# Optimization experiments

Hardware: AMD Instinct MI355X
Metric: run time of the kernel (lower is better)

Reference implementation:

```python
import jax, jax.numpy as jnp
import numpy as np
import math

N_QUBITS = 8
EMBED_DIM = 8
NUM_HEADS = 2
N_QLAYERS = 2
TWO_PI = 2.0 * math.pi


def _apply_rx(state, theta, wire):
    # state: (N,) + (2,)*n complex64; theta: scalar or (N,)
    n = state.ndim - 1
    ax = 1 + wire
    a0 = jnp.take(state, 0, axis=ax)
    a1 = jnp.take(state, 1, axis=ax)
    half = jnp.asarray(theta) * 0.5
    c = jnp.cos(half)
    s = jnp.sin(half)
    if c.ndim:  # per-sample angle -> broadcast over remaining qubit axes
        bshape = (-1,) + (1,) * (n - 1)
        c = c.reshape(bshape)
        s = s.reshape(bshape)
    js = 1j * s
    n0 = c * a0 - js * a1
    n1 = -js * a0 + c * a1
    return jnp.stack([n0, n1], axis=ax)


def _apply_cnot(state, ctrl, tgt):
    ac, at = 1 + ctrl, 1 + tgt
    s0 = jnp.take(state, 0, axis=ac)
    s1 = jnp.take(state, 1, axis=ac)
    at2 = at - 1 if at > ac else at  # target axis index after removing control axis
    s1 = jnp.flip(s1, axis=at2)
    return jnp.stack([s0, s1], axis=ac)


def qnode(inputs, weights):
    """AngleEmbedding(RX) + BasicEntanglerLayers(RX + CNOT ring), PauliZ expvals.
    inputs: (N, n) angles; weights: (L, n). Returns (N, n) expvals, fully batched."""
    N, n = inputs.shape
    L = weights.shape[0]
    state = jnp.zeros((N,) + (2,) * n, jnp.complex64)
    state = state.at[(slice(None),) + (0,) * n].set(1.0)
    for i in range(n):  # AngleEmbedding: RX(inputs[:, i]) on wire i
        state = _apply_rx(state, inputs[:, i], i)
    for l in range(L):  # BasicEntanglerLayers
        for i in range(n):
            state = _apply_rx(state, weights[l, i], i)
        for i in range(n):
            state = _apply_cnot(state, i, (i + 1) % n)
    probs = (state.real ** 2 + state.imag ** 2).reshape(N, 2 ** n)
    # wire 0 is the most significant bit of the flattened statevector index
    idx = jnp.arange(2 ** n)
    bits = (idx[:, None] >> jnp.arange(n - 1, -1, -1)[None, :]) & 1  # (2^n, n)
    signs = (1.0 - 2.0 * bits).astype(probs.dtype)
    return probs @ signs  # (N, n)


def _qproj(x, weights):
    # apply qnode to every (batch, timestep) vector at once (vectorized loop fusion)
    B, S, E = x.shape
    return qnode(x.reshape(B * S, E), weights).reshape(B, S, E)


def _attention_forward(q, k, v, wq_w, wk_w, wv_w, wd_w):
    B, S, E = q.shape
    H, D = NUM_HEADS, EMBED_DIM // NUM_HEADS
    qp = _qproj(q, wq_w)
    kp = _qproj(k, wk_w)
    vp = _qproj(v, wv_w)
    # split heads: (B, H, S, D)
    qh = qp.reshape(B, S, H, D).transpose(0, 2, 1, 3)
    kh = kp.reshape(B, S, H, D).transpose(0, 2, 1, 3)
    vh = vp.reshape(B, S, H, D).transpose(0, 2, 1, 3)
    scores = jnp.einsum('bhqd,bhkd->bhqk', qh, kh) / jnp.sqrt(jnp.asarray(D, qh.dtype))
    attn = jax.nn.softmax(scores, axis=-1)
    ctx = jnp.einsum('bhqk,bhkd->bhqd', attn, vh)
    concat = ctx.transpose(0, 2, 1, 3).reshape(B, S, E)
    out = _qproj(concat, wd_w)
    return out, attn


def setup_inputs() -> dict:
    key = jax.random.key(0)
    kq, kk, kv, k1, k2, k3, k4 = jax.random.split(key, 7)
    B, S, E = 32, 1024, EMBED_DIM
    return {
        'q': jax.random.normal(kq, (B, S, E), jnp.float32),
        'k': jax.random.normal(kk, (B, S, E), jnp.float32),
        'v': jax.random.normal(kv, (B, S, E), jnp.float32),
        'wq_weights': jax.random.uniform(k1, (N_QLAYERS, N_QUBITS), jnp.float32) * TWO_PI,
        'wk_weights': jax.random.uniform(k2, (N_QLAYERS, N_QUBITS), jnp.float32) * TWO_PI,
        'wv_weights': jax.random.uniform(k3, (N_QLAYERS, N_QUBITS), jnp.float32) * TWO_PI,
        'dense_weights': jax.random.uniform(k4, (N_QLAYERS, N_QUBITS), jnp.float32) * TWO_PI,
    }


def reference(q, k, v, wq_weights, wk_weights, wv_weights, dense_weights):
    return _attention_forward(q, k, v, wq_weights, wk_weights, wv_weights, dense_weights)
```

## Files before the change

kernel.cpp:

```cpp
#include <hip/hip_runtime.h>
#include <math.h>


#define NSAMP 32768

#define QX1 0xB1
#define QX2 0x4E
#define QX3 0x1B
#define QB0 0x00
#define QB1 0x55
#define QB2 0xAA
#define QB3 0xFF
#define ROW_MIRROR 0x140
#define ROW_HALF_MIRROR 0x141

template <int CTRL>
__device__ __forceinline__ float dppf(float x) {
  int xi = __float_as_int(x);
  return __int_as_float(
      __builtin_amdgcn_update_dpp(xi, xi, CTRL, 0xF, 0xF, false));
}

template <int ML>
__device__ __forceinline__ void gate_l(float c, float s, float* ar,
                                       float* ai) {
  constexpr int HB = ML >= 32 ? 32 : ML >= 16 ? 16 : ML >= 8 ? 8
                     : ML >= 4 ? 4 : ML >= 2 ? 2 : 1;
#pragma unroll
  for (int l = 0; l < 64; ++l) {
    if (!(l & HB)) {
      const int p = l ^ ML;
      float a0r = ar[l], a0i = ai[l], a1r = ar[p], a1i = ai[p];
      ar[l] = fmaf(c, a0r, s * a1i);
      ai[l] = fmaf(c, a0i, -s * a1r);
      ar[p] = fmaf(c, a1r, s * a0i);
      ai[p] = fmaf(c, a1i, -s * a0r);
    }
  }
}

template <int CTRL, int ML>
__device__ __forceinline__ void gate_q(float c, float s, float* ar,
                                       float* ai) {
  if constexpr (ML == 0) {
#pragma unroll
    for (int l = 0; l < 64; ++l) {
      float pr = dppf<CTRL>(ar[l]);
      float pi = dppf<CTRL>(ai[l]);
      ar[l] = fmaf(c, ar[l], s * pi);
      ai[l] = fmaf(c, ai[l], -s * pr);
    }
  } else {
    constexpr int HB = ML >= 32 ? 32 : ML >= 16 ? 16 : ML >= 8 ? 8
                       : ML >= 4 ? 4 : ML >= 2 ? 2 : 1;
#pragma unroll
    for (int l = 0; l < 64; ++l) {
      if (!(l & HB)) {
        const int p = l ^ ML;
        float prl = dppf<CTRL>(ar[p]);
        float pil = dppf<CTRL>(ai[p]);
        float prp = dppf<CTRL>(ar[l]);
        float pip = dppf<CTRL>(ai[l]);
        ar[l] = fmaf(c, ar[l], s * pil);
        ai[l] = fmaf(c, ai[l], -s * prl);
        ar[p] = fmaf(c, ar[p], s * pip);
        ai[p] = fmaf(c, ai[p], -s * prp);
      }
    }
  }
}

__device__ __forceinline__ float quad_wht(float v, int qq) {
  float u = dppf<QX1>(v);
  v = (qq & 1) ? (u - v) : (v + u);
  u = dppf<QX2>(v);
  v = (qq & 2) ? (u - v) : (v + u);
  return v;
}

__device__ __forceinline__ void qsim_wave(const float* __restrict__ in,
                                          float* __restrict__ outp,
                                          int sampBase,
                                          const float* __restrict__ wc,
                                          const float* __restrict__ wsn) {
  const int lane = threadIdx.x & 63;
  const int qq = lane & 3;
  const int g = lane >> 2;
  const int samp = sampBase + g;

  const float2 xx = *(const float2*)(in + (size_t)samp * 8 + 2 * qq);
  float h0 = 0.5f * xx.x, h1 = 0.5f * xx.y;
  float c0 = cosf(h0), s0 = sinf(h0);
  float c1 = cosf(h1), s1 = sinf(h1);
  float cw[8], sw[8];
  cw[0] = dppf<QB0>(c0); cw[1] = dppf<QB0>(c1);
  sw[0] = dppf<QB0>(s0); sw[1] = dppf<QB0>(s1);
  cw[2] = dppf<QB1>(c0); cw[3] = dppf<QB1>(c1);
  sw[2] = dppf<QB1>(s0); sw[3] = dppf<QB1>(s1);
  cw[4] = dppf<QB2>(c0); cw[5] = dppf<QB2>(c1);
  sw[4] = dppf<QB2>(s0); sw[5] = dppf<QB2>(s1);
  cw[6] = dppf<QB3>(c0); cw[7] = dppf<QB3>(c1);
  sw[6] = dppf<QB3>(s0); sw[7] = dppf<QB3>(s1);

  float ar[64], ai[64];
  ar[0] = ((qq & 1) ? sw[1] : cw[1]) * ((qq & 2) ? sw[0] : cw[0]);
#pragma unroll
  for (int k = 0; k < 6; ++k) {
    const float cc = cw[7 - k], ss = sw[7 - k];
#pragma unroll
    for (int t = (1 << k) - 1; t >= 0; --t) {
      ar[t + (1 << k)] = ar[t] * ss;
      ar[t] = ar[t] * cc;
    }
  }
  {
    const int pq = __builtin_popcount(qq);
#pragma unroll
    for (int l = 63; l >= 0; --l) {
      const int pl = __builtin_popcount(l) & 3;
      const float mm = ar[l];
      if (pl == 0) { ar[l] = mm;   ai[l] = 0.0f; }
      else if (pl == 1) { ar[l] = 0.0f; ai[l] = -mm; }
      else if (pl == 2) { ar[l] = -mm;  ai[l] = 0.0f; }
      else { ar[l] = 0.0f; ai[l] = mm; }
    }
    if (pq == 1) {
#pragma unroll
      for (int l = 0; l < 64; ++l) {
        const float t = ar[l];
        ar[l] = ai[l];
        ai[l] = -t;
      }
    } else if (pq == 2) {
#pragma unroll
      for (int l = 0; l < 64; ++l) {
        ar[l] = -ar[l];
        ai[l] = -ai[l];
      }
    }
  }

  gate_q<QX2, 0>(wc[0], wsn[0], ar, ai);
  gate_q<QX1, 0>(wc[1], wsn[1], ar, ai);
  gate_l<0x20>(wc[2], wsn[2], ar, ai);
  gate_l<0x10>(wc[3], wsn[3], ar, ai);
  gate_l<0x08>(wc[4], wsn[4], ar, ai);
  gate_l<0x04>(wc[5], wsn[5], ar, ai);
  gate_l<0x02>(wc[6], wsn[6], ar, ai);
  gate_l<0x01>(wc[7], wsn[7], ar, ai);
  gate_q<QX3, 0>(wc[8], wsn[8], ar, ai);
  gate_q<QX1, 0x20>(wc[9], wsn[9], ar, ai);
  gate_l<0x30>(wc[10], wsn[10], ar, ai);
  gate_l<0x18>(wc[11], wsn[11], ar, ai);
  gate_l<0x0C>(wc[12], wsn[12], ar, ai);
  gate_l<0x06>(wc[13], wsn[13], ar, ai);
  gate_l<0x03>(wc[14], wsn[14], ar, ai);
  gate_q<QX3, 0x01>(wc[15], wsn[15], ar, ai);

  float p[64];
#pragma unroll
  for (int l = 0; l < 64; ++l) p[l] = ar[l] * ar[l] + ai[l] * ai[l];
#pragma unroll
  for (int k = 0; k < 6; ++k) {
#pragma unroll
    for (int l = 0; l < 64; ++l) {
      if (!(l & (1 << k))) {
        const int q2 = l | (1 << k);
        const float a = p[l], b = p[q2];
        p[l] = a + b;
        p[q2] = a - b;
      }
    }
  }
  const float o15 = quad_wht(p[0x15], qq);
  const float o3F = quad_wht(p[0x3F], qq);
  const float o1F = quad_wht(p[0x1F], qq);
  const float o2F = quad_wht(p[0x2F], qq);
  const float o17 = quad_wht(p[0x17], qq);
  const float o2B = quad_wht(p[0x2B], qq);
  const float o2A = quad_wht(p[0x2A], qq);

  float* orow = outp + (size_t)samp * 8;
  if (qq == 3) orow[0] = o15;
  if (qq == 2) {
    orow[1] = o3F;
    orow[3] = o2F;
    orow[5] = o2B;
    orow[7] = o2A;
  }
  if (qq == 1) {
    orow[2] = o1F;
    orow[4] = o17;
    orow[6] = o15;
  }
}

__device__ __forceinline__ void weight_trig(const float* __restrict__ w,
                                            float* __restrict__ tc,
                                            float* __restrict__ tsn) {
  if (threadIdx.x < 32) {
    const int a = threadIdx.x & 15;
    const float half = 0.5f * w[a];
    if (threadIdx.x < 16)
      tc[a] = cosf(half);
    else
      tsn[a] = sinf(half);
  }
  __syncthreads();
}

__global__ __launch_bounds__(256, 2) void mhaq_qproj3_kernel(
    const float* __restrict__ q, const float* __restrict__ k,
    const float* __restrict__ v, const float* __restrict__ wq,
    const float* __restrict__ wk, const float* __restrict__ wv,
    float* __restrict__ qp, float* __restrict__ kp, float* __restrict__ vp) {
  __shared__ float tc[16], tsn[16];
  const int wg = blockIdx.x * 4 + (threadIdx.x >> 6);
  const int proj = wg >> 11;
  const float* wsel = proj == 0 ? wq : proj == 1 ? wk : wv;
  weight_trig(wsel, tc, tsn);
  const float* in = proj == 0 ? q : proj == 1 ? k : v;
  float* op = proj == 0 ? qp : proj == 1 ? kp : vp;
  qsim_wave(in, op, (wg & 2047) * 16, tc, tsn);
}

__global__ __launch_bounds__(256, 2) void mhaq_qproj1_kernel(
    const float* __restrict__ ctx, const float* __restrict__ wd,
    float* __restrict__ outp) {
  __shared__ float tc[16], tsn[16];
  weight_trig(wd, tc, tsn);
  const int wg = blockIdx.x * 4 + (threadIdx.x >> 6);
  qsim_wave(ctx, outp, wg * 16, tc, tsn);
}

__device__ __forceinline__ float wred_sum(float v) {
  v += dppf<QX1>(v);
  v += dppf<QX2>(v);
  v += dppf<ROW_HALF_MIRROR>(v);
  v += dppf<ROW_MIRROR>(v);
  v += __shfl_xor(v, 16, 64);
  v += __shfl_xor(v, 32, 64);
  return v;
}
__device__ __forceinline__ float wred_max(float v) {
  v = fmaxf(v, dppf<QX1>(v));
  v = fmaxf(v, dppf<QX2>(v));
  v = fmaxf(v, dppf<ROW_HALF_MIRROR>(v));
  v = fmaxf(v, dppf<ROW_MIRROR>(v));
  v = fmaxf(v, __shfl_xor(v, 16, 64));
  v = fmaxf(v, __shfl_xor(v, 32, 64));
  return v;
}

__global__ __launch_bounds__(256, 2) void mhaq_attn_kernel(
    const float* __restrict__ qp, const float* __restrict__ kp,
    const float* __restrict__ vp, float* __restrict__ ctx,
    float* __restrict__ attn) {
  const int wg = blockIdx.x * 4 + (threadIdx.x >> 6);
  const int bh = wg >> 7;
  const int chunk = wg & 127;
  const int b = bh >> 1, h = bh & 1;
  const int lane = threadIdx.x & 63;

  float4 kreg[16], vreg[16];
  const float* kbase = kp + (size_t)b * 1024 * 8 + h * 4;
  const float* vbase = vp + (size_t)b * 1024 * 8 + h * 4;
#pragma unroll
  for (int t = 0; t < 4; ++t) {
#pragma unroll
    for (int c = 0; c < 4; ++c) {
      const size_t j = (size_t)t * 256 + lane * 4 + c;
      kreg[t * 4 + c] = *(const float4*)(kbase + j * 8);
      vreg[t * 4 + c] = *(const float4*)(vbase + j * 8);
    }
  }

  for (int r = 0; r < 8; ++r) {
    const int i = chunk * 8 + r;
    const float4 qv = *(const float4*)(qp + ((size_t)b * 1024 + i) * 8 + h * 4);
    float e[16];
    float mx = -1e30f;
#pragma unroll
    for (int t = 0; t < 16; ++t) {
      float s = qv.x * kreg[t].x + qv.y * kreg[t].y + qv.z * kreg[t].z +
                qv.w * kreg[t].w;
      s *= 0.5f;
      e[t] = s;
      mx = fmaxf(mx, s);
    }
    mx = wred_max(mx);
    float sum = 0.0f;
#pragma unroll
    for (int t = 0; t < 16; ++t) {
      e[t] = __expf(e[t] - mx);
      sum += e[t];
    }
    sum = wred_sum(sum);
    const float rinv = 1.0f / sum;

    float a0 = 0.f, a1 = 0.f, a2 = 0.f, a3 = 0.f;
    float* arow = attn + ((size_t)(bh * 1024 + i)) * 1024;
#pragma unroll
    for (int t = 0; t < 4; ++t) {
      float p0 = e[4 * t] * rinv, p1 = e[4 * t + 1] * rinv,
            p2 = e[4 * t + 2] * rinv, p3 = e[4 * t + 3] * rinv;
      *(float4*)(arow + t * 256 + lane * 4) = make_float4(p0, p1, p2, p3);
      a0 = fmaf(p0, vreg[4 * t].x, a0);
      a1 = fmaf(p0, vreg[4 * t].y, a1);
      a2 = fmaf(p0, vreg[4 * t].z, a2);
      a3 = fmaf(p0, vreg[4 * t].w, a3);
      a0 = fmaf(p1, vreg[4 * t + 1].x, a0);
      a1 = fmaf(p1, vreg[4 * t + 1].y, a1);
      a2 = fmaf(p1, vreg[4 * t + 1].z, a2);
      a3 = fmaf(p1, vreg[4 * t + 1].w, a3);
      a0 = fmaf(p2, vreg[4 * t + 2].x, a0);
      a1 = fmaf(p2, vreg[4 * t + 2].y, a1);
      a2 = fmaf(p2, vreg[4 * t + 2].z, a2);
      a3 = fmaf(p2, vreg[4 * t + 2].w, a3);
      a0 = fmaf(p3, vreg[4 * t + 3].x, a0);
      a1 = fmaf(p3, vreg[4 * t + 3].y, a1);
      a2 = fmaf(p3, vreg[4 * t + 3].z, a2);
      a3 = fmaf(p3, vreg[4 * t + 3].w, a3);
    }
    a0 = wred_sum(a0);
    a1 = wred_sum(a1);
    a2 = wred_sum(a2);
    a3 = wred_sum(a3);
    if (lane == 0)
      *(float4*)(ctx + ((size_t)b * 1024 + i) * 8 + h * 4) =
          make_float4(a0, a1, a2, a3);
  }
}

extern "C" void kernel_launch(void* const* d_in, const int* in_sizes, int n_in,
                              void* d_out, int out_size, void* d_ws,
                              size_t ws_size, hipStream_t stream) {
  (void)in_sizes; (void)n_in; (void)out_size; (void)ws_size;
  const float* q = (const float*)d_in[0];
  const float* k = (const float*)d_in[1];
  const float* v = (const float*)d_in[2];
  const float* wq = (const float*)d_in[3];
  const float* wk = (const float*)d_in[4];
  const float* wv = (const float*)d_in[5];
  const float* wd = (const float*)d_in[6];
  float* outp = (float*)d_out;
  float* attn = outp + 262144;

  float* wsf = (float*)d_ws;
  float* qp = wsf;
  float* kp = qp + (size_t)NSAMP * 8;
  float* vp = kp + (size_t)NSAMP * 8;
  float* ctx = vp + (size_t)NSAMP * 8;

  hipLaunchKernelGGL(mhaq_qproj3_kernel, dim3(1536), dim3(256), 0, stream, q,
                     k, v, wq, wk, wv, qp, kp, vp);
  hipLaunchKernelGGL(mhaq_attn_kernel, dim3(2048), dim3(256), 0, stream, qp,
                     kp, vp, ctx, attn);
  hipLaunchKernelGGL(mhaq_qproj1_kernel, dim3(512), dim3(256), 0, stream, ctx,
                     wd, outp);
}
```

Measured before the change: 385.5 us.

## Pack statevector into float2 pairs for packed FMA and prune the Walsh-Hadamard

Stores the per-lane 64-amplitude statevector as 32 float2 pairs, with the lowest local qubit held inside each pair, so gate updates can use packed FP32 FMA instructions (v_pk_fma_f32). Gates on that qubit become in-pair swaps. The final Walsh-Hadamard reduction is cut to 3 stages per group of eight, and only the seven needed output coefficients are built explicitly. This is meant to halve the VALU instruction count, at the cost of extra swizzle moves and possible register-allocation changes.

After: 364.7 us. 1.06x faster.

```diff
diff --git a/kernel.cpp b/kernel.cpp
--- a/kernel.cpp
+++ b/kernel.cpp
@@ -3,6 +3,8 @@
 
 
 #define NSAMP 32768
+
+typedef float f2 __attribute__((ext_vector_type(2)));
 
 #define QX1 0xB1
 #define QX2 0x4E
@@ -21,51 +23,101 @@
       __builtin_amdgcn_update_dpp(xi, xi, CTRL, 0xF, 0xF, false));
 }
 
+template <int CTRL>
+__device__ __forceinline__ f2 dpp2(f2 v) {
+  f2 r;
+  r.x = dppf<CTRL>(v.x);
+  r.y = dppf<CTRL>(v.y);
+  return r;
+}
+
+__device__ __forceinline__ f2 swap2(f2 v) {
+  f2 r;
+  r.x = v.y;
+  r.y = v.x;
+  return r;
+}
+
+#define F2FMA(a, b, c) __builtin_elementwise_fma((a), (b), (c))
+
+
+template <int CTRL>
+__device__ __forceinline__ void gq0(float c, float s, f2* vr, f2* vi) {
+  const f2 c2 = {c, c}, s2 = {s, s};
+#pragma unroll
+  for (int m = 0; m < 32; ++m) {
+    f2 pr = dpp2<CTRL>(vr[m]);
+    f2 pi = dpp2<CTRL>(vi[m]);
+    vr[m] = F2FMA(c2, vr[m], s2 * pi);
+    vi[m] = F2FMA(c2, vi[m], -s2 * pr);
+  }
+}
+
+template <int CTRL>
+__device__ __forceinline__ void gq_l1(float c, float s, f2* vr, f2* vi) {
+  const f2 c2 = {c, c}, s2 = {s, s};
+#pragma unroll
+  for (int m = 0; m < 32; m += 2) {
+    f2 pr0 = dpp2<CTRL>(vr[m]), pi0 = dpp2<CTRL>(vi[m]);
+    f2 pr1 = dpp2<CTRL>(vr[m + 1]), pi1 = dpp2<CTRL>(vi[m + 1]);
+    vr[m] = F2FMA(c2, vr[m], s2 * pi1);
+    vi[m] = F2FMA(c2, vi[m], -s2 * pr1);
+    vr[m + 1] = F2FMA(c2, vr[m + 1], s2 * pi0);
+    vi[m + 1] = F2FMA(c2, vi[m + 1], -s2 * pr0);
+  }
+}
+
+template <int CTRL>
+__device__ __forceinline__ void gq_l20(float c, float s, f2* vr, f2* vi) {
+  const f2 c2 = {c, c}, s2 = {s, s};
+#pragma unroll
+  for (int m = 0; m < 32; ++m) {
+    f2 pr = dpp2<CTRL>(vr[m]);
+    f2 pi = dpp2<CTRL>(vi[m]);
+    vr[m] = F2FMA(c2, vr[m], s2 * swap2(pi));
+    vi[m] = F2FMA(c2, vi[m], -s2 * swap2(pr));
+  }
+}
+
 template <int ML>
-__device__ __forceinline__ void gate_l(float c, float s, float* ar,
-                                       float* ai) {
-  constexpr int HB = ML >= 32 ? 32 : ML >= 16 ? 16 : ML >= 8 ? 8
-                     : ML >= 4 ? 4 : ML >= 2 ? 2 : 1;
-#pragma unroll
-  for (int l = 0; l < 64; ++l) {
-    if (!(l & HB)) {
-      const int p = l ^ ML;
-      float a0r = ar[l], a0i = ai[l], a1r = ar[p], a1i = ai[p];
-      ar[l] = fmaf(c, a0r, s * a1i);
-      ai[l] = fmaf(c, a0i, -s * a1r);
-      ar[p] = fmaf(c, a1r, s * a0i);
-      ai[p] = fmaf(c, a1i, -s * a0r);
-    }
-  }
-}
-
-template <int CTRL, int ML>
-__device__ __forceinline__ void gate_q(float c, float s, float* ar,
-                                       float* ai) {
-  if constexpr (ML == 0) {
-#pragma unroll
-    for (int l = 0; l < 64; ++l) {
-      float pr = dppf<CTRL>(ar[l]);
-      float pi = dppf<CTRL>(ai[l]);
-      ar[l] = fmaf(c, ar[l], s * pi);
-      ai[l] = fmaf(c, ai[l], -s * pr);
-    }
-  } else {
-    constexpr int HB = ML >= 32 ? 32 : ML >= 16 ? 16 : ML >= 8 ? 8
-                       : ML >= 4 ? 4 : ML >= 2 ? 2 : 1;
-#pragma unroll
-    for (int l = 0; l < 64; ++l) {
-      if (!(l & HB)) {
-        const int p = l ^ ML;
-        float prl = dppf<CTRL>(ar[p]);
-        float pil = dppf<CTRL>(ai[p]);
-        float prp = dppf<CTRL>(ar[l]);
-        float pip = dppf<CTRL>(ai[l]);
-        ar[l] = fmaf(c, ar[l], s * pil);
-        ai[l] = fmaf(c, ai[l], -s * prl);
-        ar[p] = fmaf(c, ar[p], s * pip);
-        ai[p] = fmaf(c, ai[p], -s * prp);
-      }
+__device__ __forceinline__ void gl(float c, float s, f2* vr, f2* vi) {
+  constexpr int HB = ML >= 16 ? 16 : ML >= 8 ? 8 : ML >= 4 ? 4
+                     : ML >= 2 ? 2 : 1;
+  const f2 c2 = {c, c}, s2 = {s, s};
+#pragma unroll
+  for (int m = 0; m < 32; ++m) {
+    if (!(m & HB)) {
+      const int p = m ^ ML;
+      f2 a0r = vr[m], a0i = vi[m], a1r = vr[p], a1i = vi[p];
+      vr[m] = F2FMA(c2, a0r, s2 * a1i);
+      vi[m] = F2FMA(c2, a0i, -s2 * a1r);
+      vr[p] = F2FMA(c2, a1r, s2 * a0i);
+      vi[p] = F2FMA(c2, a1i, -s2 * a0r);
+    }
+  }
+}
+
+__device__ __forceinline__ void gl20(float c, float s, f2* vr, f2* vi) {
+  const f2 c2 = {c, c}, s2 = {s, s};
+#pragma unroll
+  for (int m = 0; m < 32; ++m) {
+    f2 orr = vr[m], oii = vi[m];
+    vr[m] = F2FMA(c2, orr, s2 * swap2(oii));
+    vi[m] = F2FMA(c2, oii, -s2 * swap2(orr));
+  }
+}
+
+__device__ __forceinline__ void gl30(float c, float s, f2* vr, f2* vi) {
+  const f2 c2 = {c, c}, s2 = {s, s};
+#pragma unroll
+  for (int m = 0; m < 32; ++m) {
+    if (!(m & 0x10)) {
+      const int p = m ^ 0x10;
+      f2 or0 = vr[m], oi0 = vi[m], or1 = vr[p], oi1 = vi[p];
+      vr[m] = F2FMA(c2, or0, s2 * swap2(oi1));
+      vi[m] = F2FMA(c2, oi0, -s2 * swap2(or1));
+      vr[p] = F2FMA(c2, or1, s2 * swap2(oi0));
+      vi[p] = F2FMA(c2, oi1, -s2 * swap2(or0));
     }
   }
 }
@@ -102,83 +154,105 @@
   cw[6] = dppf<QB3>(c0); cw[7] = dppf<QB3>(c1);
   sw[6] = dppf<QB3>(s0); sw[7] = dppf<QB3>(s1);
 
-  float ar[64], ai[64];
-  ar[0] = ((qq & 1) ? sw[1] : cw[1]) * ((qq & 2) ? sw[0] : cw[0]);
-#pragma unroll
-  for (int k = 0; k < 6; ++k) {
+  float mm[32];
+  mm[0] = ((qq & 1) ? sw[1] : cw[1]) * ((qq & 2) ? sw[0] : cw[0]);
+#pragma unroll
+  for (int k = 0; k < 5; ++k) {
     const float cc = cw[7 - k], ss = sw[7 - k];
 #pragma unroll
     for (int t = (1 << k) - 1; t >= 0; --t) {
-      ar[t + (1 << k)] = ar[t] * ss;
-      ar[t] = ar[t] * cc;
-    }
-  }
-  {
-    const int pq = __builtin_popcount(qq);
-#pragma unroll
-    for (int l = 63; l >= 0; --l) {
-      const int pl = __builtin_popcount(l) & 3;
-      const float mm = ar[l];
-      if (pl == 0) { ar[l] = mm;   ai[l] = 0.0f; }
-      else if (pl == 1) { ar[l] = 0.0f; ai[l] = -mm; }
-      else if (pl == 2) { ar[l] = -mm;  ai[l] = 0.0f; }
-      else { ar[l] = 0.0f; ai[l] = mm; }
-    }
-    if (pq == 1) {
-#pragma unroll
-      for (int l = 0; l < 64; ++l) {
-        const float t = ar[l];
-        ar[l] = ai[l];
-        ai[l] = -t;
+      mm[t + (1 << k)] = mm[t] * ss;
+      mm[t] = mm[t] * cc;
+    }
+  }
+
+  f2 vr[32], vi[32];
+  const int pq = __builtin_popcount(qq);
+#pragma unroll
+  for (int m = 0; m < 32; ++m) {
+    const float mx = mm[m] * cw[2];
+    const float my = mm[m] * sw[2];
+    const int plx = __builtin_popcount(m) & 3;
+    f2 r, i;
+    if (plx == 0) { r.x = mx;    i.x = 0.0f;  r.y = 0.0f;  i.y = -my; }
+    else if (plx == 1) { r.x = 0.0f; i.x = -mx; r.y = -my; i.y = 0.0f; }
+    else if (plx == 2) { r.x = -mx; i.x = 0.0f; r.y = 0.0f; i.y = my; }
+    else { r.x = 0.0f; i.x = mx;   r.y = my;   i.y = 0.0f; }
+    vr[m] = r;
+    vi[m] = i;
+  }
+  if (pq == 1) {
+#pragma unroll
+    for (int m = 0; m < 32; ++m) {
+      f2 t = vr[m];
+      vr[m] = vi[m];
+      vi[m] = -t;
+    }
+  } else if (pq == 2) {
+#pragma unroll
+    for (int m = 0; m < 32; ++m) {
+      vr[m] = -vr[m];
+      vi[m] = -vi[m];
+    }
+  }
+
+  gq0<QX2>(wc[0], wsn[0], vr, vi);
+  gq0<QX1>(wc[1], wsn[1], vr, vi);
+  gl20(wc[2], wsn[2], vr, vi);
+  gl<0x10>(wc[3], wsn[3], vr, vi);
+  gl<0x08>(wc[4], wsn[4], vr, vi);
+  gl<0x04>(wc[5], wsn[5], vr, vi);
+  gl<0x02>(wc[6], wsn[6], vr, vi);
+  gl<0x01>(wc[7], wsn[7], vr, vi);
+  gq0<QX3>(wc[8], wsn[8], vr, vi);
+  gq_l20<QX1>(wc[9], wsn[9], vr, vi);
+  gl30(wc[10], wsn[10], vr, vi);
+  gl<0x18>(wc[11], wsn[11], vr, vi);
+  gl<0x0C>(wc[12], wsn[12], vr, vi);
+  gl<0x06>(wc[13], wsn[13], vr, vi);
+  gl<0x03>(wc[14], wsn[14], vr, vi);
+  gq_l1<QX3>(wc[15], wsn[15], vr, vi);
+
+  f2 wv[32];
+#pragma unroll
+  for (int m = 0; m < 32; ++m)
+    wv[m] = F2FMA(vr[m], vr[m], vi[m] * vi[m]);
+#pragma unroll
+  for (int gi = 0; gi < 4; ++gi) {
+#pragma unroll
+    for (int k = 0; k < 3; ++k) {
+#pragma unroll
+      for (int j = 0; j < 8; ++j) {
+        if (!(j & (1 << k))) {
+          const int a = gi * 8 + j, b2 = a | (1 << k);
+          f2 A = wv[a], B = wv[b2];
+          wv[a] = A + B;
+          wv[b2] = A - B;
+        }
       }
-    } else if (pq == 2) {
-#pragma unroll
-      for (int l = 0; l < 64; ++l) {
-        ar[l] = -ar[l];
-        ai[l] = -ai[l];
-      }
-    }
-  }
-
-  gate_q<QX2, 0>(wc[0], wsn[0], ar, ai);
-  gate_q<QX1, 0>(wc[1], wsn[1], ar, ai);
-  gate_l<0x20>(wc[2], wsn[2], ar, ai);
-  gate_l<0x10>(wc[3], wsn[3], ar, ai);
-  gate_l<0x08>(wc[4], wsn[4], ar, ai);
-  gate_l<0x04>(wc[5], wsn[5], ar, ai);
-  gate_l<0x02>(wc[6], wsn[6], ar, ai);
-  gate_l<0x01>(wc[7], wsn[7], ar, ai);
-  gate_q<QX3, 0>(wc[8], wsn[8], ar, ai);
-  gate_q<QX1, 0x20>(wc[9], wsn[9], ar, ai);
-  gate_l<0x30>(wc[10], wsn[10], ar, ai);
-  gate_l<0x18>(wc[11], wsn[11], ar, ai);
-  gate_l<0x0C>(wc[12], wsn[12], ar, ai);
-  gate_l<0x06>(wc[13], wsn[13], ar, ai);
-  gate_l<0x03>(wc[14], wsn[14], ar, ai);
-  gate_q<QX3, 0x01>(wc[15], wsn[15], ar, ai);
-
-  float p[64];
-#pragma unroll
-  for (int l = 0; l < 64; ++l) p[l] = ar[l] * ar[l] + ai[l] * ai[l];
-#pragma unroll
-  for (int k = 0; k < 6; ++k) {
-#pragma unroll
-    for (int l = 0; l < 64; ++l) {
-      if (!(l & (1 << k))) {
-        const int q2 = l | (1 << k);
-        const float a = p[l], b = p[q2];
-        p[l] = a + b;
-        p[q2] = a - b;
-      }
-    }
-  }
-  const float o15 = quad_wht(p[0x15], qq);
-  const float o3F = quad_wht(p[0x3F], qq);
-  const float o1F = quad_wht(p[0x1F], qq);
-  const float o2F = quad_wht(p[0x2F], qq);
-  const float o17 = quad_wht(p[0x17], qq);
-  const float o2B = quad_wht(p[0x2B], qq);
-  const float o2A = quad_wht(p[0x2A], qq);
+    }
+  }
+  const f2 aA = (wv[5] + wv[13]) - (wv[21] + wv[29]);
+  const f2 aBC = (wv[7] + wv[31]) - (wv[15] + wv[23]);
+  const f2 aD = (wv[7] + wv[23]) - (wv[15] + wv[31]);
+  const f2 aE = (wv[7] + wv[15]) - (wv[23] + wv[31]);
+  const f2 aF = (wv[3] + wv[19]) - (wv[11] + wv[27]);
+  const f2 aG = (wv[2] + wv[18]) - (wv[10] + wv[26]);
+  const float accA = aA.x + aA.y;
+  const float accB = aBC.x - aBC.y;
+  const float accC = aBC.x + aBC.y;
+  const float accD = aD.x - aD.y;
+  const float accE = aE.x + aE.y;
+  const float accF = aF.x - aF.y;
+  const float accG = aG.x - aG.y;
+
+  const float o15 = quad_wht(accA, qq);
+  const float o3F = quad_wht(accB, qq);
+  const float o1F = quad_wht(accC, qq);
+  const float o2F = quad_wht(accD, qq);
+  const float o17 = quad_wht(accE, qq);
+  const float o2B = quad_wht(accF, qq);
+  const float o2A = quad_wht(accG, qq);
 
   float* orow = outp + (size_t)samp * 8;
   if (qq == 3) orow[0] = o15;
```
